# Kernel optimization log

Measured on AMD Instinct MI355X. Metric: run time of the kernel, lower is better.

The kernel has to match this reference:

```python
import jax, jax.numpy as jnp
import numpy as np

EPS = 0.1
TANH_SCALE = 1.0
B, T, N, D, C, DE = 8, 120, 24, 48, 1128, 256  # C = D*(D-1)//2


def setup_inputs() -> dict:
    key = jax.random.key(0)
    k1, k2, k3, k4 = jax.random.split(key, 4)
    x = jax.random.normal(k1, (B, T, N, D), dtype=jnp.float32)
    context = jax.random.normal(k2, (B, C, N, DE), dtype=jnp.float32)
    Wkv = jax.random.normal(k3, (D, DE), dtype=jnp.float32) * (DE ** -0.5)
    bkv = jax.random.normal(k4, (D,), dtype=jnp.float32) * 0.01
    return {"x": x, "context": context, "Wkv": Wkv, "bkv": bkv}


def reference(x, context, Wkv, bkv):
    # x: [B,T,N,D], context: [B,C,N,DE]
    b, t, n, d = x.shape
    kv = jnp.einsum('bcne,de->bcnd', context, Wkv) + bkv      # [B,C,N,D]
    kv = jnp.transpose(kv, (0, 2, 3, 1))                      # [B,N,D,C]
    xt = jnp.transpose(x, (0, 2, 1, 3))                       # [B,N,T,D]
    sp = jnp.einsum('bntd,bndc->bntc', xt, kv)                # [B,N,T,C]
    sp = EPS * TANH_SCALE * jnp.tanh(sp / TANH_SCALE)
    i, j = jnp.tril_indices(d, k=-1)
    A = jnp.zeros((b, n, t, d, d), dtype=x.dtype).at[..., i, j].set(sp)
    A = A - jnp.swapaxes(A, -1, -2)                           # skew-symmetric
    dx = jnp.einsum('bntd,bntde->bnte', xt, A)                # per-(B,N,T) matvec
    y = xt + dx
    return jnp.transpose(y, (0, 2, 1, 3))                     # [B,T,N,D]
```

## Files before the change

### kernel.cpp

```cpp
#include <hip/hip_runtime.h>
#include <hip/hip_bf16.h>


constexpr int Bc = 8, Tc = 120, Nc = 24, Dc = 48, Cc = 1128, DEc = 256;
constexpr int BNc = Bc * Nc;
constexpr int KVP = 64;

using short8 = __attribute__((ext_vector_type(8))) short;
using f32x4  = __attribute__((ext_vector_type(4))) float;

__device__ __forceinline__ ushort f2b(float f) {
    union { float f; unsigned u; } v; v.f = f;
    unsigned r = (v.u + 0x7fffu + ((v.u >> 16) & 1u)) >> 16;
    return (ushort)r;
}
__device__ __forceinline__ short bcast(float f) {
    return (short)__bfloat16_as_ushort(__float2bfloat16(f));
}
__device__ __forceinline__ short8 pack8(const float4& a, const float4& b) {
    short8 r;
    r[0] = bcast(a.x); r[1] = bcast(a.y); r[2] = bcast(a.z); r[3] = bcast(a.w);
    r[4] = bcast(b.x); r[5] = bcast(b.y); r[6] = bcast(b.z); r[7] = bcast(b.w);
    return r;
}

__global__ void k0w(const float* __restrict__ Wkv, ushort* __restrict__ wkvb) {
    int i = blockIdx.x * 256 + threadIdx.x;
    float4 w = *reinterpret_cast<const float4*>(Wkv + i * 4);
    ushort4 u;
    u.x = (ushort)bcast(w.x); u.y = (ushort)bcast(w.y);
    u.z = (ushort)bcast(w.z); u.w = (ushort)bcast(w.w);
    *reinterpret_cast<ushort4*>(wkvb + i * 4) = u;
}

constexpr int SWs = 264;
__global__ __launch_bounds__(256) void k1_kv(const float* __restrict__ ctx,
                                             const ushort* __restrict__ wkvb,
                                             const float* __restrict__ bkv,
                                             ushort* __restrict__ kvb) {
    __shared__ ushort sW[Dc * SWs];
    const int bn = blockIdx.x, c0 = blockIdx.y * 128;
    const int b = bn / Nc, n = bn % Nc;
    const int tid = threadIdx.x, wave = tid >> 6, lane = tid & 63;
    const int tr = lane & 15, kg = lane >> 4;
    const float* ctxb = ctx + ((size_t)b * Cc * Nc + n) * DEc;

    for (int l = tid; l < Dc * 32; l += 256) {
        int d = l >> 5, e = (l & 31) << 3;
        *reinterpret_cast<short8*>(&sW[d * SWs + e]) =
            *reinterpret_cast<const short8*>(&wkvb[d * DEc + e]);
    }

    const float* crow[2];
    #pragma unroll
    for (int cn = 0; cn < 2; ++cn) {
        int c = c0 + wave * 32 + cn * 16 + tr;
        crow[cn] = ctxb + (size_t)(c < Cc ? c : Cc - 1) * (Nc * DEc);
    }

    f32x4 acc[3][2];
    #pragma unroll
    for (int mf = 0; mf < 3; ++mf)
        #pragma unroll
        for (int cn = 0; cn < 2; ++cn) acc[mf][cn] = (f32x4){0.f, 0.f, 0.f, 0.f};

    __syncthreads();

    #pragma unroll
    for (int ks = 0; ks < 8; ++ks) {
        const int e0 = ks * 32 + kg * 8;
        short8 bfrag[2];
        #pragma unroll
        for (int cn = 0; cn < 2; ++cn) {
            float4 a0 = *reinterpret_cast<const float4*>(crow[cn] + e0);
            float4 a1 = *reinterpret_cast<const float4*>(crow[cn] + e0 + 4);
            bfrag[cn] = pack8(a0, a1);
        }
        short8 afrag[3];
        #pragma unroll
        for (int mf = 0; mf < 3; ++mf)
            afrag[mf] = *reinterpret_cast<const short8*>(&sW[(mf * 16 + tr) * SWs + e0]);
        #pragma unroll
        for (int mf = 0; mf < 3; ++mf)
            #pragma unroll
            for (int cn = 0; cn < 2; ++cn)
                acc[mf][cn] = __builtin_amdgcn_mfma_f32_16x16x32_bf16(afrag[mf], bfrag[cn], acc[mf][cn], 0, 0, 0);
    }

    float4 bias[3];
    #pragma unroll
    for (int mf = 0; mf < 3; ++mf)
        bias[mf] = *reinterpret_cast<const float4*>(bkv + mf * 16 + kg * 4);
    #pragma unroll
    for (int cn = 0; cn < 2; ++cn) {
        int c = c0 + wave * 32 + cn * 16 + tr;
        if (c < Cc) {
            ushort* dst = kvb + ((size_t)bn * Cc + c) * KVP;
            #pragma unroll
            for (int mf = 0; mf < 3; ++mf) {
                ushort4 u;
                u.x = f2b(acc[mf][cn][0] + bias[mf].x);
                u.y = f2b(acc[mf][cn][1] + bias[mf].y);
                u.z = f2b(acc[mf][cn][2] + bias[mf].z);
                u.w = f2b(acc[mf][cn][3] + bias[mf].w);
                *reinterpret_cast<ushort4*>(dst + mf * 16 + kg * 4) = u;
            }
        }
    }
    {
        int row = lane >> 1, half = lane & 1;
        int c = c0 + wave * 32 + row;
        if (c < Cc) {
            short8 z = (short8){0, 0, 0, 0, 0, 0, 0, 0};
            *reinterpret_cast<short8*>(&kvb[((size_t)bn * Cc + c) * KVP + 48 + half * 8]) = z;
        }
    }
}

constexpr int SGs = 1136;
__global__ __launch_bounds__(256) void k2_fused(const float* __restrict__ x,
                                                const ushort* __restrict__ kvb,
                                                float* __restrict__ out) {
    __shared__ float  sG[16 * SGs];
    __shared__ float  sXf[16 * 52];
    __shared__ ushort sXb[16 * 72];
    const int L = blockIdx.x;
    const int bn = (L & 7) + 8 * (L >> 6);
    const int tt = (L >> 3) & 7;
    const int b = bn / Nc, n = bn % Nc, t0 = tt * 16;
    const int tid = threadIdx.x, wave = tid >> 6, lane = tid & 63;
    const int tr = lane & 15, kg = lane >> 4;

    for (int l = tid; l < 16 * 72 / 4; l += 256)
        *reinterpret_cast<ushort4*>(&sXb[l * 4]) = make_ushort4(0, 0, 0, 0);
    __syncthreads();
    if (tid < 192) {
        int t = tid / 12, dv = (tid % 12) * 4, tg = t0 + t;
        float4 v = make_float4(0.f, 0.f, 0.f, 0.f);
        if (tg < Tc) v = *reinterpret_cast<const float4*>(x + (((size_t)b * Tc + tg) * Nc + n) * Dc + dv);
        *reinterpret_cast<float4*>(&sXf[t * 52 + dv]) = v;
        *reinterpret_cast<ushort4*>(&sXb[t * 72 + dv]) = make_ushort4(f2b(v.x), f2b(v.y), f2b(v.z), f2b(v.w));
    }
    __syncthreads();
    const short8 af0 = *reinterpret_cast<const short8*>(&sXb[tr * 72 + kg * 8]);
    const short8 af1 = *reinterpret_cast<const short8*>(&sXb[tr * 72 + 32 + kg * 8]);
    const ushort* kvbn = kvb + (size_t)bn * Cc * KVP;
    for (int nf = wave; nf < 71; nf += 4) {
        int c = nf * 16 + tr;
        int ce = c < Cc ? c : Cc - 1;
        short8 b0 = *reinterpret_cast<const short8*>(&kvbn[(size_t)ce * KVP + kg * 8]);
        short8 b1 = *reinterpret_cast<const short8*>(&kvbn[(size_t)ce * KVP + 32 + kg * 8]);
        f32x4 a = (f32x4){0.f, 0.f, 0.f, 0.f};
        a = __builtin_amdgcn_mfma_f32_16x16x32_bf16(af0, b0, a, 0, 0, 0);
        a = __builtin_amdgcn_mfma_f32_16x16x32_bf16(af1, b1, a, 0, 0, 0);
        #pragma unroll
        for (int r = 0; r < 4; ++r) {
            float g = 0.1f - 0.2f * __builtin_amdgcn_rcpf(__expf(2.0f * a[r]) + 1.0f);
            sG[(kg * 4 + r) * SGs + c] = g;
        }
    }
    __syncthreads();
    int ea[3], ta[3], tea[3];
    float dxa[3];
    #pragma unroll
    for (int p = 0; p < 3; ++p) {
        int idx = tid + p * 256;
        ta[p] = idx / 48; ea[p] = idx % 48;
        tea[p] = ea[p] * (ea[p] - 1) / 2;
        dxa[p] = 0.f;
    }
    int td = 0;
    #pragma unroll 4
    for (int d = 0; d < 48; ++d) {
        #pragma unroll
        for (int p = 0; p < 3; ++p) {
            bool gt = d > ea[p];
            int c = gt ? (td + ea[p]) : (tea[p] + d);
            float gv = sG[ta[p] * SGs + c];
            float xv = sXf[ta[p] * 52 + d];
            float m = gt ? xv : -xv;
            if (d == ea[p]) m = 0.f;
            dxa[p] = fmaf(m, gv, dxa[p]);
        }
        td += d;
    }
    #pragma unroll
    for (int p = 0; p < 3; ++p) {
        int tg = t0 + ta[p];
        if (tg < Tc)
            out[(((size_t)b * Tc + tg) * Nc + n) * Dc + ea[p]] = sXf[ta[p] * 52 + ea[p]] + dxa[p];
    }
}

extern "C" void kernel_launch(void* const* d_in, const int* in_sizes, int n_in,
                              void* d_out, int out_size, void* d_ws, size_t ws_size,
                              hipStream_t stream) {
    (void)in_sizes; (void)n_in; (void)out_size; (void)ws_size;
    const float* x   = (const float*)d_in[0];
    const float* ctx = (const float*)d_in[1];
    const float* Wkv = (const float*)d_in[2];
    const float* bkv = (const float*)d_in[3];
    float* out   = (float*)d_out;
    ushort* wkvb = (ushort*)d_ws;
    ushort* kvb  = (ushort*)((char*)d_ws + 32768);

    k0w<<<dim3(12), dim3(256), 0, stream>>>(Wkv, wkvb);
    k1_kv<<<dim3(BNc, 9), dim3(256), 0, stream>>>(ctx, wkvb, bkv, kvb);
    k2_fused<<<dim3(BNc * 8), dim3(256), 0, stream>>>(x, kvb, out);
}
```

Before: 97.58 us.

## Flatten kv projection over contiguous context rows and prefetch next K-slice

The kv projection kernel now tiles over the flattened (b,c,n) row index, so each block reads 128 contiguous context rows instead of rows strided by N*DE. This gives sequential DRAM access and removes the tail-block waste from C not dividing 128. The output row is scattered back to the [b,n,c] kv layout with per-row index arithmetic. The loop also register-double-buffers the next K-slice of context loads, which raises register pressure.

```diff
diff --git a/kernel.cpp b/kernel.cpp
--- a/kernel.cpp
+++ b/kernel.cpp
@@ -5,6 +5,7 @@
 constexpr int Bc = 8, Tc = 120, Nc = 24, Dc = 48, Cc = 1128, DEc = 256;
 constexpr int BNc = Bc * Nc;
 constexpr int KVP = 64;
+constexpr int Mtot = Bc * Cc * Nc;
 
 using short8 = __attribute__((ext_vector_type(8))) short;
 using f32x4  = __attribute__((ext_vector_type(4))) float;
@@ -39,11 +40,9 @@
                                              const float* __restrict__ bkv,
                                              ushort* __restrict__ kvb) {
     __shared__ ushort sW[Dc * SWs];
-    const int bn = blockIdx.x, c0 = blockIdx.y * 128;
-    const int b = bn / Nc, n = bn % Nc;
     const int tid = threadIdx.x, wave = tid >> 6, lane = tid & 63;
     const int tr = lane & 15, kg = lane >> 4;
-    const float* ctxb = ctx + ((size_t)b * Cc * Nc + n) * DEc;
+    const int r0 = blockIdx.x * 128;
 
     for (int l = tid; l < Dc * 32; l += 256) {
         int d = l >> 5, e = (l & 31) << 3;
@@ -51,11 +50,12 @@
             *reinterpret_cast<const short8*>(&wkvb[d * DEc + e]);
     }
 
-    const float* crow[2];
+    int rr[2];
+    const float* rowp[2];
     #pragma unroll
     for (int cn = 0; cn < 2; ++cn) {
-        int c = c0 + wave * 32 + cn * 16 + tr;
-        crow[cn] = ctxb + (size_t)(c < Cc ? c : Cc - 1) * (Nc * DEc);
+        rr[cn] = r0 + wave * 32 + cn * 16 + tr;
+        rowp[cn] = ctx + (size_t)rr[cn] * DEc + kg * 8;
     }
 
     f32x4 acc[3][2];
@@ -64,27 +64,40 @@
         #pragma unroll
         for (int cn = 0; cn < 2; ++cn) acc[mf][cn] = (f32x4){0.f, 0.f, 0.f, 0.f};
 
+    float4 cur[2][2], nxt[2][2];
+    #pragma unroll
+    for (int cn = 0; cn < 2; ++cn) {
+        cur[cn][0] = *reinterpret_cast<const float4*>(rowp[cn]);
+        cur[cn][1] = *reinterpret_cast<const float4*>(rowp[cn] + 4);
+    }
     __syncthreads();
 
     #pragma unroll
     for (int ks = 0; ks < 8; ++ks) {
-        const int e0 = ks * 32 + kg * 8;
+        if (ks < 7) {
+            #pragma unroll
+            for (int cn = 0; cn < 2; ++cn) {
+                nxt[cn][0] = *reinterpret_cast<const float4*>(rowp[cn] + (ks + 1) * 32);
+                nxt[cn][1] = *reinterpret_cast<const float4*>(rowp[cn] + (ks + 1) * 32 + 4);
+            }
+        }
         short8 bfrag[2];
         #pragma unroll
-        for (int cn = 0; cn < 2; ++cn) {
-            float4 a0 = *reinterpret_cast<const float4*>(crow[cn] + e0);
-            float4 a1 = *reinterpret_cast<const float4*>(crow[cn] + e0 + 4);
-            bfrag[cn] = pack8(a0, a1);
-        }
+        for (int cn = 0; cn < 2; ++cn) bfrag[cn] = pack8(cur[cn][0], cur[cn][1]);
         short8 afrag[3];
         #pragma unroll
         for (int mf = 0; mf < 3; ++mf)
-            afrag[mf] = *reinterpret_cast<const short8*>(&sW[(mf * 16 + tr) * SWs + e0]);
+            afrag[mf] = *reinterpret_cast<const short8*>(&sW[(mf * 16 + tr) * SWs + ks * 32 + kg * 8]);
         #pragma unroll
         for (int mf = 0; mf < 3; ++mf)
             #pragma unroll
             for (int cn = 0; cn < 2; ++cn)
                 acc[mf][cn] = __builtin_amdgcn_mfma_f32_16x16x32_bf16(afrag[mf], bfrag[cn], acc[mf][cn], 0, 0, 0);
+        #pragma unroll
+        for (int cn = 0; cn < 2; ++cn) {
+            cur[cn][0] = nxt[cn][0];
+            cur[cn][1] = nxt[cn][1];
+        }
     }
 
     float4 bias[3];
@@ -93,26 +106,24 @@
         bias[mf] = *reinterpret_cast<const float4*>(bkv + mf * 16 + kg * 4);
     #pragma unroll
     for (int cn = 0; cn < 2; ++cn) {
-        int c = c0 + wave * 32 + cn * 16 + tr;
-        if (c < Cc) {
-            ushort* dst = kvb + ((size_t)bn * Cc + c) * KVP;
-            #pragma unroll
-            for (int mf = 0; mf < 3; ++mf) {
-                ushort4 u;
-                u.x = f2b(acc[mf][cn][0] + bias[mf].x);
-                u.y = f2b(acc[mf][cn][1] + bias[mf].y);
-                u.z = f2b(acc[mf][cn][2] + bias[mf].z);
-                u.w = f2b(acc[mf][cn][3] + bias[mf].w);
-                *reinterpret_cast<ushort4*>(dst + mf * 16 + kg * 4) = u;
-            }
-        }
-    }
-    {
-        int row = lane >> 1, half = lane & 1;
-        int c = c0 + wave * 32 + row;
-        if (c < Cc) {
+        int r = rr[cn];
+        int b = r / (Cc * Nc);
+        int rem = r - b * (Cc * Nc);
+        int c = rem / Nc;
+        int n = rem - c * Nc;
+        ushort* dst = kvb + (((size_t)(b * Nc + n)) * Cc + c) * KVP;
+        #pragma unroll
+        for (int mf = 0; mf < 3; ++mf) {
+            ushort4 u;
+            u.x = f2b(acc[mf][cn][0] + bias[mf].x);
+            u.y = f2b(acc[mf][cn][1] + bias[mf].y);
+            u.z = f2b(acc[mf][cn][2] + bias[mf].z);
+            u.w = f2b(acc[mf][cn][3] + bias[mf].w);
+            *reinterpret_cast<ushort4*>(dst + mf * 16 + kg * 4) = u;
+        }
+        if (kg < 2) {
             short8 z = (short8){0, 0, 0, 0, 0, 0, 0, 0};
-            *reinterpret_cast<short8*>(&kvb[((size_t)bn * Cc + c) * KVP + 48 + half * 8]) = z;
+            *reinterpret_cast<short8*>(dst + 48 + kg * 8) = z;
         }
     }
 }
@@ -205,6 +216,6 @@
     ushort* kvb  = (ushort*)((char*)d_ws + 32768);
 
     k0w<<<dim3(12), dim3(256), 0, stream>>>(Wkv, wkvb);
-    k1_kv<<<dim3(BNc, 9), dim3(256), 0, stream>>>(ctx, wkvb, bkv, kvb);
+    k1_kv<<<dim3(Mtot / 128), dim3(256), 0, stream>>>(ctx, wkvb, bkv, kvb);
     k2_fused<<<dim3(BNc * 8), dim3(256), 0, stream>>>(x, kvb, out);
 }
```

Result: slower. 101.2 us (+3.7%).

## Build dense skew matrix in LDS and use 8-token tiles in fused kernel

Applied to the files above, without the earlier changes.

The fused kernel now scatters the tanh-scaled scores as bf16 into a dense per-token 48x48 skew-symmetric matrix in shared memory, finding the (i,j) index with a sqrt-based inverse. The final matvec then reads contiguous 8-wide vectors instead of doing branchy triangular gathers. Token tiles shrink from 16 to 8, so blocks go from 1536 to 2880, but the MFMA still computes 16 rows and half of them are thrown away. The stored coefficients are rounded to bf16, which lowers precision, and the MFMA-to-kv load work per output roughly doubles.

```diff
diff --git a/kernel.cpp b/kernel.cpp
--- a/kernel.cpp
+++ b/kernel.cpp
@@ -117,31 +117,38 @@
     }
 }
 
-constexpr int SGs = 1136;
+constexpr int TT = 8;
+constexpr int MTs = 56;
+constexpr int MTt = 2696;
 __global__ __launch_bounds__(256) void k2_fused(const float* __restrict__ x,
                                                 const ushort* __restrict__ kvb,
                                                 float* __restrict__ out) {
-    __shared__ float  sG[16 * SGs];
-    __shared__ float  sXf[16 * 52];
+    __shared__ ushort sM[TT * MTt];
+    __shared__ float  sXf[TT * 52];
     __shared__ ushort sXb[16 * 72];
     const int L = blockIdx.x;
-    const int bn = (L & 7) + 8 * (L >> 6);
-    const int tt = (L >> 3) & 7;
-    const int b = bn / Nc, n = bn % Nc, t0 = tt * 16;
+    const int slot = L & 7, idx = L >> 3;
+    const int bn = slot * 24 + idx / 15;
+    const int tt = idx % 15;
+    const int b = bn / Nc, n = bn % Nc, t0 = tt * TT;
     const int tid = threadIdx.x, wave = tid >> 6, lane = tid & 63;
     const int tr = lane & 15, kg = lane >> 4;
 
-    for (int l = tid; l < 16 * 72 / 4; l += 256)
-        *reinterpret_cast<ushort4*>(&sXb[l * 4]) = make_ushort4(0, 0, 0, 0);
-    __syncthreads();
-    if (tid < 192) {
+    for (int l = tid; l < 144; l += 256)
+        *reinterpret_cast<short8*>(&sXb[l * 8]) = (short8){0,0,0,0,0,0,0,0};
+    for (int l = tid; l < TT * Dc; l += 256) {
+        int t = l / Dc, d = l - t * Dc;
+        sM[t * MTt + d * MTs + d] = 0;
+    }
+    __syncthreads();
+    if (tid < TT * 12) {
         int t = tid / 12, dv = (tid % 12) * 4, tg = t0 + t;
-        float4 v = make_float4(0.f, 0.f, 0.f, 0.f);
-        if (tg < Tc) v = *reinterpret_cast<const float4*>(x + (((size_t)b * Tc + tg) * Nc + n) * Dc + dv);
+        float4 v = *reinterpret_cast<const float4*>(x + (((size_t)b * Tc + tg) * Nc + n) * Dc + dv);
         *reinterpret_cast<float4*>(&sXf[t * 52 + dv]) = v;
         *reinterpret_cast<ushort4*>(&sXb[t * 72 + dv]) = make_ushort4(f2b(v.x), f2b(v.y), f2b(v.z), f2b(v.w));
     }
     __syncthreads();
+
     const short8 af0 = *reinterpret_cast<const short8*>(&sXb[tr * 72 + kg * 8]);
     const short8 af1 = *reinterpret_cast<const short8*>(&sXb[tr * 72 + 32 + kg * 8]);
     const ushort* kvbn = kvb + (size_t)bn * Cc * KVP;
@@ -153,42 +160,53 @@
         f32x4 a = (f32x4){0.f, 0.f, 0.f, 0.f};
         a = __builtin_amdgcn_mfma_f32_16x16x32_bf16(af0, b0, a, 0, 0, 0);
         a = __builtin_amdgcn_mfma_f32_16x16x32_bf16(af1, b1, a, 0, 0, 0);
+        int i = (int)((1.0f + sqrtf(1.0f + 8.0f * (float)c)) * 0.5f);
+        while (i * (i - 1) / 2 > c) --i;
+        while ((i + 1) * i / 2 <= c) ++i;
+        int j = c - i * (i - 1) / 2;
+        const bool cok = (c < Cc);
         #pragma unroll
         for (int r = 0; r < 4; ++r) {
+            int t = kg * 4 + r;
             float g = 0.1f - 0.2f * __builtin_amdgcn_rcpf(__expf(2.0f * a[r]) + 1.0f);
-            sG[(kg * 4 + r) * SGs + c] = g;
-        }
-    }
-    __syncthreads();
-    int ea[3], ta[3], tea[3];
-    float dxa[3];
-    #pragma unroll
-    for (int p = 0; p < 3; ++p) {
-        int idx = tid + p * 256;
-        ta[p] = idx / 48; ea[p] = idx % 48;
-        tea[p] = ea[p] * (ea[p] - 1) / 2;
-        dxa[p] = 0.f;
-    }
-    int td = 0;
-    #pragma unroll 4
-    for (int d = 0; d < 48; ++d) {
-        #pragma unroll
-        for (int p = 0; p < 3; ++p) {
-            bool gt = d > ea[p];
-            int c = gt ? (td + ea[p]) : (tea[p] + d);
-            float gv = sG[ta[p] * SGs + c];
-            float xv = sXf[ta[p] * 52 + d];
-            float m = gt ? xv : -xv;
-            if (d == ea[p]) m = 0.f;
-            dxa[p] = fmaf(m, gv, dxa[p]);
-        }
-        td += d;
-    }
-    #pragma unroll
-    for (int p = 0; p < 3; ++p) {
-        int tg = t0 + ta[p];
-        if (tg < Tc)
-            out[(((size_t)b * Tc + tg) * Nc + n) * Dc + ea[p]] = sXf[ta[p] * 52 + ea[p]] + dxa[p];
+            ushort gb = f2b(g);
+            if (cok && t < TT) {
+                sM[t * MTt + j * MTs + i] = gb;
+                sM[t * MTt + i * MTs + j] = (ushort)(gb ^ 0x8000u);
+            }
+        }
+    }
+    __syncthreads();
+
+    float xr[48];
+    {
+        int t = tid & 7;
+        #pragma unroll
+        for (int v = 0; v < 12; ++v) {
+            float4 w = *reinterpret_cast<const float4*>(&sXf[t * 52 + v * 4]);
+            xr[v * 4 + 0] = w.x; xr[v * 4 + 1] = w.y;
+            xr[v * 4 + 2] = w.z; xr[v * 4 + 3] = w.w;
+        }
+    }
+    #pragma unroll
+    for (int pp = 0; pp < 2; ++pp) {
+        int pidx = tid + pp * 256;
+        if (pidx < TT * Dc) {
+            int t = tid & 7, e = pidx >> 3;
+            float dx = 0.f;
+            #pragma unroll
+            for (int v = 0; v < 6; ++v) {
+                short8 a8 = *reinterpret_cast<const short8*>(&sM[t * MTt + e * MTs + v * 8]);
+                #pragma unroll
+                for (int u = 0; u < 8; ++u) {
+                    union { unsigned q; float f; } cv;
+                    cv.q = ((unsigned)(ushort)a8[u]) << 16;
+                    dx = fmaf(xr[v * 8 + u], cv.f, dx);
+                }
+            }
+            int tg = t0 + t;
+            out[(((size_t)b * Tc + tg) * Nc + n) * Dc + e] = sXf[t * 52 + e] + dx;
+        }
     }
 }
 
@@ -206,5 +224,5 @@
 
     k0w<<<dim3(12), dim3(256), 0, stream>>>(Wkv, wkvb);
     k1_kv<<<dim3(BNc, 9), dim3(256), 0, stream>>>(ctx, wkvb, bkv, kvb);
-    k2_fused<<<dim3(BNc * 8), dim3(256), 0, stream>>>(x, kvb, out);
-}
+    k2_fused<<<dim3(BNc * 15), dim3(256), 0, stream>>>(x, kvb, out);
+}
```

Result: slower. 123.3 us (+26.4%).

## Store tanh gate in bf16 LDS, prefetch kv fragments, remap matvec threads

Applied to the files above, without the earlier changes.

The gate matrix in shared memory is now stored as bf16 instead of fp32. This roughly halves LDS use per block, so three blocks can fit per CU, which the launch bounds now request. The kv fragment loads are software-pipelined with a one-step register prefetch across a fully unrolled loop. The matvec phase is remapped so each thread handles one t row and three e columns, caching the x row in registers to avoid repeated LDS reads. Rounding the gate to bf16 adds extra rounding error, and the register-held x row raises register pressure.

```diff
diff --git a/kernel.cpp b/kernel.cpp
--- a/kernel.cpp
+++ b/kernel.cpp
@@ -13,6 +13,9 @@
     union { float f; unsigned u; } v; v.f = f;
     unsigned r = (v.u + 0x7fffu + ((v.u >> 16) & 1u)) >> 16;
     return (ushort)r;
+}
+__device__ __forceinline__ float b2f(ushort u) {
+    union { unsigned q; float f; } cv; cv.q = ((unsigned)u) << 16; return cv.f;
 }
 __device__ __forceinline__ short bcast(float f) {
     return (short)__bfloat16_as_ushort(__float2bfloat16(f));
@@ -117,11 +120,11 @@
     }
 }
 
-constexpr int SGs = 1136;
-__global__ __launch_bounds__(256) void k2_fused(const float* __restrict__ x,
-                                                const ushort* __restrict__ kvb,
-                                                float* __restrict__ out) {
-    __shared__ float  sG[16 * SGs];
+constexpr int SG2 = 1140;
+__global__ __launch_bounds__(256, 3) void k2_fused(const float* __restrict__ x,
+                                                   const ushort* __restrict__ kvb,
+                                                   float* __restrict__ out) {
+    __shared__ ushort sG[16 * SG2];
     __shared__ float  sXf[16 * 52];
     __shared__ ushort sXb[16 * 72];
     const int L = blockIdx.x;
@@ -133,6 +136,8 @@
 
     for (int l = tid; l < 16 * 72 / 4; l += 256)
         *reinterpret_cast<ushort4*>(&sXb[l * 4]) = make_ushort4(0, 0, 0, 0);
+    for (int l = tid; l < 16 * 12; l += 256)
+        sG[(l / 12) * SG2 + 1128 + (l % 12)] = 0;
     __syncthreads();
     if (tid < 192) {
         int t = tid / 12, dv = (tid % 12) * 4, tg = t0 + t;
@@ -144,51 +149,83 @@
     __syncthreads();
     const short8 af0 = *reinterpret_cast<const short8*>(&sXb[tr * 72 + kg * 8]);
     const short8 af1 = *reinterpret_cast<const short8*>(&sXb[tr * 72 + 32 + kg * 8]);
+
     const ushort* kvbn = kvb + (size_t)bn * Cc * KVP;
-    for (int nf = wave; nf < 71; nf += 4) {
-        int c = nf * 16 + tr;
-        int ce = c < Cc ? c : Cc - 1;
-        short8 b0 = *reinterpret_cast<const short8*>(&kvbn[(size_t)ce * KVP + kg * 8]);
-        short8 b1 = *reinterpret_cast<const short8*>(&kvbn[(size_t)ce * KVP + 32 + kg * 8]);
-        f32x4 a = (f32x4){0.f, 0.f, 0.f, 0.f};
-        a = __builtin_amdgcn_mfma_f32_16x16x32_bf16(af0, b0, a, 0, 0, 0);
-        a = __builtin_amdgcn_mfma_f32_16x16x32_bf16(af1, b1, a, 0, 0, 0);
-        #pragma unroll
-        for (int r = 0; r < 4; ++r) {
-            float g = 0.1f - 0.2f * __builtin_amdgcn_rcpf(__expf(2.0f * a[r]) + 1.0f);
-            sG[(kg * 4 + r) * SGs + c] = g;
-        }
-    }
-    __syncthreads();
-    int ea[3], ta[3], tea[3];
-    float dxa[3];
+    short8 cb0[2], cb1[2], nb0[2], nb1[2];
+    #pragma unroll
+    for (int q = 0; q < 2; ++q) {
+        int c = (wave * 2 + q) * 16 + tr;
+        const ushort* p = kvbn + (size_t)c * KVP + kg * 8;
+        cb0[q] = *reinterpret_cast<const short8*>(p);
+        cb1[q] = *reinterpret_cast<const short8*>(p + 32);
+    }
+    #pragma unroll
+    for (int u = 0; u < 9; ++u) {
+        if (u < 8) {
+            #pragma unroll
+            for (int q = 0; q < 2; ++q) {
+                int c = ((u + 1) * 8 + wave * 2 + q) * 16 + tr;
+                if (c > Cc - 1) c = Cc - 1;
+                const ushort* p = kvbn + (size_t)c * KVP + kg * 8;
+                nb0[q] = *reinterpret_cast<const short8*>(p);
+                nb1[q] = *reinterpret_cast<const short8*>(p + 32);
+            }
+        }
+        #pragma unroll
+        for (int q = 0; q < 2; ++q) {
+            f32x4 a = (f32x4){0.f, 0.f, 0.f, 0.f};
+            a = __builtin_amdgcn_mfma_f32_16x16x32_bf16(af0, cb0[q], a, 0, 0, 0);
+            a = __builtin_amdgcn_mfma_f32_16x16x32_bf16(af1, cb1[q], a, 0, 0, 0);
+            int c = (u * 8 + wave * 2 + q) * 16 + tr;
+            if (c < Cc) {
+                #pragma unroll
+                for (int r = 0; r < 4; ++r) {
+                    float g = 0.1f - 0.2f * __builtin_amdgcn_rcpf(__expf(2.0f * a[r]) + 1.0f);
+                    sG[(kg * 4 + r) * SG2 + c] = f2b(g);
+                }
+            }
+        }
+        #pragma unroll
+        for (int q = 0; q < 2; ++q) { cb0[q] = nb0[q]; cb1[q] = nb1[q]; }
+    }
+    __syncthreads();
+
+    const int tb = tid & 15, eg = tid >> 4;
+    float xr[48];
+    #pragma unroll
+    for (int v = 0; v < 12; ++v) {
+        float4 w = *reinterpret_cast<const float4*>(&sXf[tb * 52 + v * 4]);
+        xr[v * 4 + 0] = w.x; xr[v * 4 + 1] = w.y;
+        xr[v * 4 + 2] = w.z; xr[v * 4 + 3] = w.w;
+    }
+    float dxa[3]; int ep[3], te[3];
     #pragma unroll
     for (int p = 0; p < 3; ++p) {
-        int idx = tid + p * 256;
-        ta[p] = idx / 48; ea[p] = idx % 48;
-        tea[p] = ea[p] * (ea[p] - 1) / 2;
+        ep[p] = eg * 3 + p;
+        te[p] = ep[p] * (ep[p] - 1) / 2;
         dxa[p] = 0.f;
     }
+    const ushort* grow = &sG[tb * SG2];
     int td = 0;
-    #pragma unroll 4
+    #pragma unroll 8
     for (int d = 0; d < 48; ++d) {
+        float xv = xr[d];
         #pragma unroll
         for (int p = 0; p < 3; ++p) {
-            bool gt = d > ea[p];
-            int c = gt ? (td + ea[p]) : (tea[p] + d);
-            float gv = sG[ta[p] * SGs + c];
-            float xv = sXf[ta[p] * 52 + d];
+            bool gt = d > ep[p];
+            int c = gt ? (td + ep[p]) : (te[p] + d);
+            float gv = b2f(grow[c]);
             float m = gt ? xv : -xv;
-            if (d == ea[p]) m = 0.f;
+            if (d == ep[p]) m = 0.f;
             dxa[p] = fmaf(m, gv, dxa[p]);
         }
         td += d;
     }
-    #pragma unroll
-    for (int p = 0; p < 3; ++p) {
-        int tg = t0 + ta[p];
-        if (tg < Tc)
-            out[(((size_t)b * Tc + tg) * Nc + n) * Dc + ea[p]] = sXf[ta[p] * 52 + ea[p]] + dxa[p];
+    int tg = t0 + tb;
+    if (tg < Tc) {
+        #pragma unroll
+        for (int p = 0; p < 3; ++p)
+            out[(((size_t)b * Tc + tg) * Nc + n) * Dc + ep[p]] = sXf[tb * 52 + ep[p]] + dxa[p];
     }
 }
 
```

After: 112.4 us. 15.2% more time.
